# Kernel tuning notes

Measured on AMD Instinct MI355X. Metric: run time of the kernel, lower is better.

## Reference

```python
import jax, jax.numpy as jnp
import numpy as np

N = 100000
E = 1250000
D = 64
R = 16


def _glorot(key, shape):
    fan_in, fan_out = shape[-2], shape[-1]
    lim = jnp.sqrt(6.0 / (fan_in + fan_out))
    return jax.random.uniform(key, shape, jnp.float32, -lim, lim)


def setup_inputs() -> dict:
    key = jax.random.key(0)
    ks = jax.random.split(key, 9)
    x = jax.random.normal(ks[0], (N, D), jnp.float32)
    edge_index = jax.random.randint(ks[1], (2, E), 0, N, jnp.int64 if jax.config.jax_enable_x64 else jnp.int32).astype(jnp.int32)
    edge_type = jax.random.randint(ks[2], (E,), 0, R).astype(jnp.int32)
    return {
        "x": x,
        "edge_index": edge_index,
        "edge_type": edge_type,
        "W1": _glorot(ks[3], (R, D, D)),
        "sw1": _glorot(ks[4], (D, D)),
        "b1": jnp.zeros((D,), jnp.float32),
        "W2": _glorot(ks[5], (R, D, D)),
        "sw2": _glorot(ks[6], (D, D)),
        "b2": jnp.zeros((D,), jnp.float32),
    }


def _rgcn_layer(x, src, dst, edge_type, W, sw, b, residual):
    # self transform [N, O]
    out = x @ sw
    # per-relation transform of all nodes: [N, R, O] (avoids [E, D, O] gathered weights,
    # same math as bmm(x_j, W[edge_type]))
    xW = jnp.einsum('nd,rdo->nro', x, W)
    msg = xW[src, edge_type]                      # [E, O] per-edge messages
    agg = jax.ops.segment_sum(msg, dst, num_segments=N)  # scatter-add aggregate
    out = out + agg
    if residual:
        out = out + x  # Identity residual (in == out channels)
    out = out + b
    return jax.nn.relu(out)


def reference(x, edge_index, edge_type, W1, sw1, b1, W2, sw2, b2):
    src, dst = edge_index[0], edge_index[1]
    # layer 1: residual=True; layer 2: encoding=False -> no residual.
    # activation (relu) applied after every layer by RGCN.forward; dropout p=0 / eval -> no-op.
    h = _rgcn_layer(x, src, dst, edge_type, W1, sw1, b1, residual=True)
    h = _rgcn_layer(h, src, dst, edge_type, W2, sw2, b2, residual=False)
    return h
```

## Files before the change

### kernel.cpp

```cpp
#include <hip/hip_runtime.h>
#include <hip/hip_bf16.h>

#define NN 100000
#define NE 1250000
#define DD 64
#define RR 16
#define NTILE 6250
#define NBINS 100000
#define NBLK_SCAN 391
#define EBCAP 512
#define CLCAP 24

typedef __attribute__((ext_vector_type(8))) short s16x8;
typedef __attribute__((ext_vector_type(4))) float f32x4;

static __device__ __forceinline__ unsigned short f2bf(float v) {
    __hip_bfloat16 h = __float2bfloat16(v);
    return __builtin_bit_cast(unsigned short, h);
}
static __device__ __forceinline__ unsigned int pack2(float a, float b) {
    return ((unsigned int)f2bf(b) << 16) | (unsigned int)f2bf(a);
}


__global__ void hist_key(const int* __restrict__ dst, const int* __restrict__ et,
                         int* __restrict__ cnt) {
    int e = blockIdx.x * 256 + threadIdx.x;
    if (e < NE) atomicAdd(&cnt[(dst[e] >> 4) * 16 + et[e]], 1);
}

__global__ __launch_bounds__(256) void scan1(const int* __restrict__ cnt,
                                             int* __restrict__ rp, int* __restrict__ part) {
    __shared__ int s[256];
    int i = blockIdx.x * 256 + threadIdx.x;
    int v = (i < NBINS) ? cnt[i] : 0;
    s[threadIdx.x] = v;
    __syncthreads();
    for (int off = 1; off < 256; off <<= 1) {
        int t = (threadIdx.x >= off) ? s[threadIdx.x - off] : 0;
        __syncthreads();
        s[threadIdx.x] += t;
        __syncthreads();
    }
    if (i < NBINS) rp[i] = s[threadIdx.x] - v;
    if (threadIdx.x == 255) part[blockIdx.x] = s[255];
}

__global__ void scan2(int* __restrict__ part, int* __restrict__ rp) {
    __shared__ int s[NBLK_SCAN];
    if (threadIdx.x < NBLK_SCAN) s[threadIdx.x] = part[threadIdx.x];
    __syncthreads();
    if (threadIdx.x == 0) {
        int acc = 0;
        for (int b = 0; b < NBLK_SCAN; ++b) { int t = s[b]; s[b] = acc; acc += t; }
        rp[NBINS] = NE;
    }
    __syncthreads();
    if (threadIdx.x < NBLK_SCAN) part[threadIdx.x] = s[threadIdx.x];
}

__global__ void scan3(int* __restrict__ rp, const int* __restrict__ part, int* __restrict__ cur) {
    int i = blockIdx.x * 256 + threadIdx.x;
    if (i < NBINS) {
        int v = rp[i] + part[blockIdx.x];
        rp[i] = v;
        cur[i] = v;
    }
}

__global__ void scatter_key(const int* __restrict__ src, const int* __restrict__ dst,
                            const int* __restrict__ et, int* __restrict__ cur,
                            unsigned int* __restrict__ ep) {
    int e = blockIdx.x * 256 + threadIdx.x;
    if (e >= NE) return;
    int d = dst[e];
    int p = atomicAdd(&cur[(d >> 4) * 16 + et[e]], 1);
    ep[p] = (unsigned int)src[e] | ((unsigned int)(d & 15) << 20);
}


__global__ void prep_w2(const float* __restrict__ W1, const float* __restrict__ sw1,
                        const float* __restrict__ W2, const float* __restrict__ sw2,
                        unsigned short* __restrict__ wt) {
    int i = blockIdx.x * 256 + threadIdx.x;
    if (i >= 2 * 17 * DD * DD) return;
    int d = i & 63;
    int o = (i >> 6) & 63;
    int p = (i >> 12) % 17;
    int l = i / (17 * DD * DD);
    const float* srcp;
    if (p < 16) srcp = (l ? W2 : W1) + p * DD * DD;
    else        srcp = (l ? sw2 : sw1);
    wt[i] = f2bf(srcp[d * DD + o]);
}

__global__ void prep_x2(const float* __restrict__ x, unsigned short* __restrict__ xb) {
    int i = blockIdx.x * blockDim.x + threadIdx.x;
    if (i < NN * DD) xb[i] = f2bf(x[i]);
}


static __device__ __forceinline__ void load_chunk(
    const unsigned short* __restrict__ xb,
    const unsigned int* __restrict__ esrc, int ebase,
    int b0, int s1, int c, int q,
    s16x8& aA0, s16x8& aA1, s16x8& aB0, s16x8& aB1,
    int& dlA, int& dlB, bool& hasB)
{
    hasB = (s1 - b0) > 16;
    int eA = min(b0 + c, s1 - 1);
    unsigned int wa = esrc[eA - ebase];
    int srcA = (int)(wa & 0xFFFFF);
    dlA = (b0 + c < s1) ? (int)(wa >> 20) : 31;
    const unsigned short* xrA = xb + (size_t)srcA * DD + q * 8;
    aA0 = *(const s16x8*)(xrA);
    aA1 = *(const s16x8*)(xrA + 32);
    dlB = 31;
    if (hasB) {
        int eB = min(b0 + 16 + c, s1 - 1);
        unsigned int wb = esrc[eB - ebase];
        int srcB = (int)(wb & 0xFFFFF);
        dlB = (b0 + 16 + c < s1) ? (int)(wb >> 20) : 31;
        const unsigned short* xrB = xb + (size_t)srcB * DD + q * 8;
        aB0 = *(const s16x8*)(xrB);
        aB1 = *(const s16x8*)(xrB + 32);
    } else {
        aB0 = aA0;
        aB1 = aA1;
    }
}

static __device__ __forceinline__ void compute_chunk4(
    const unsigned short* __restrict__ wt, int r, int c, int q,
    const s16x8& aA0, const s16x8& aA1, const s16x8& aB0, const s16x8& aB1,
    int dlA, int dlB, bool hasB, f32x4* D)
{
    s16x8 a2;
    #pragma unroll
    for (int j = 0; j < 4; ++j) {
        int dj = __shfl(dlA, q * 4 + j, 64);
        a2[j] = (dj == c) ? (short)0x3F80 : (short)0;
    }
    #pragma unroll
    for (int j = 0; j < 4; ++j) {
        int dj = hasB ? __shfl(dlB, q * 4 + j, 64) : 31;
        a2[j + 4] = (dj == c) ? (short)0x3F80 : (short)0;
    }
    #pragma unroll
    for (int ob = 0; ob < 4; ++ob) {
        const unsigned short* wrow = wt + r * (DD * DD) + (ob * 16 + c) * DD + q * 8;
        s16x8 w0 = *(const s16x8*)(wrow);
        s16x8 w1 = *(const s16x8*)(wrow + 32);
        f32x4 cA = {0.f, 0.f, 0.f, 0.f};
        cA = __builtin_amdgcn_mfma_f32_16x16x32_bf16(aA0, w0, cA, 0, 0, 0);
        cA = __builtin_amdgcn_mfma_f32_16x16x32_bf16(aA1, w1, cA, 0, 0, 0);
        s16x8 b2;
        if (hasB) {
            f32x4 cB = {0.f, 0.f, 0.f, 0.f};
            cB = __builtin_amdgcn_mfma_f32_16x16x32_bf16(aB0, w0, cB, 0, 0, 0);
            cB = __builtin_amdgcn_mfma_f32_16x16x32_bf16(aB1, w1, cB, 0, 0, 0);
            #pragma unroll
            for (int j = 0; j < 4; ++j) {
                b2[j]     = (short)f2bf(cA[j]);
                b2[j + 4] = (short)f2bf(cB[j]);
            }
        } else {
            #pragma unroll
            for (int j = 0; j < 4; ++j) {
                b2[j]     = (short)f2bf(cA[j]);
                b2[j + 4] = 0;
            }
        }
        D[ob] = __builtin_amdgcn_mfma_f32_16x16x32_bf16(a2, b2, D[ob], 0, 0, 0);
    }
}

__global__ __launch_bounds__(256) void fused_layer(
    const unsigned short* __restrict__ xb,
    const unsigned short* __restrict__ wt,
    const int* __restrict__ rp,
    const unsigned int* __restrict__ ep,
    const float* __restrict__ bias,
    const float* __restrict__ xres,
    unsigned short* __restrict__ outb,
    float* __restrict__ outf)
{
    __shared__ unsigned int eb[EBCAP];
    __shared__ int rps[17];
    __shared__ float Dred[4 * 1024];
    __shared__ int clist[4][CLCAP];
    __shared__ int cmeta[4][3];
    const int tid  = threadIdx.x;
    const int wid  = tid >> 6;
    const int lane = tid & 63;
    const int c = lane & 15;
    const int q = lane >> 4;
    const int tile = blockIdx.x;
    const int n0 = tile * 16;

    const int e0 = rp[tile * 16];
    const int cnt = rp[tile * 16 + 16] - e0;
    if (tid < 17) rps[tid] = rp[tile * 16 + tid];
    const bool inLds = (cnt <= EBCAP);
    {
        const int nst = min(cnt, EBCAP);
        for (int i = tid; i < nst; i += 256) eb[i] = ep[e0 + i];
    }
    __syncthreads();

    if (lane == 0) {
        int m = 0;
        int ovr = -1, ovb = 0;
        for (int rr = wid; rr < 16 && ovr < 0; rr += 4) {
            for (int b0 = rps[rr]; b0 < rps[rr + 1]; b0 += 32) {
                if (m < CLCAP) clist[wid][m++] = (rr << 27) | (b0 - e0);
                else { ovr = rr; ovb = b0; break; }
            }
        }
        cmeta[wid][0] = m;
        cmeta[wid][1] = ovr;
        cmeta[wid][2] = ovb;
    }
    __syncthreads();

    const unsigned int* esrc = inLds ? eb : (ep + e0);
    f32x4 D[4];
    #pragma unroll
    for (int ob = 0; ob < 4; ++ob) D[ob] = (f32x4){0.f, 0.f, 0.f, 0.f};
    const int m = cmeta[wid][0];

    s16x8 aA0, aA1, aB0, aB1;
    int dlA = 31, dlB = 31;
    bool hB = false;
    int rC = 0;
    if (m > 0) {
        int meta = clist[wid][0];
        rC = meta >> 27;
        int b0 = e0 + (meta & 0x7FFFFFF);
        load_chunk(xb, esrc, e0, b0, rps[rC + 1], c, q, aA0, aA1, aB0, aB1, dlA, dlB, hB);
    }
    for (int ci = 0; ci < m; ++ci) {
        s16x8 nA0, nA1, nB0, nB1;
        int ndlA = 31, ndlB = 31;
        bool nhB = false;
        int rN = 0;
        if (ci + 1 < m) {
            int meta = clist[wid][ci + 1];
            rN = meta >> 27;
            int b0 = e0 + (meta & 0x7FFFFFF);
            load_chunk(xb, esrc, e0, b0, rps[rN + 1], c, q, nA0, nA1, nB0, nB1, ndlA, ndlB, nhB);
        }
        compute_chunk4(wt, rC, c, q, aA0, aA1, aB0, aB1, dlA, dlB, hB, D);
        aA0 = nA0; aA1 = nA1; aB0 = nB0; aB1 = nB1;
        dlA = ndlA; dlB = ndlB; hB = nhB; rC = rN;
    }

    {
        const int orr = cmeta[wid][1];
        if (orr >= 0) {
            for (int rr = orr; rr < 16; rr += 4) {
                const int bst = (rr == orr) ? cmeta[wid][2] : rps[rr];
                const int s1 = rps[rr + 1];
                for (int b0 = bst; b0 < s1; b0 += 32) {
                    s16x8 tA0, tA1, tB0, tB1;
                    int tdlA, tdlB;
                    bool thB;
                    load_chunk(xb, esrc, e0, b0, s1, c, q, tA0, tA1, tB0, tB1, tdlA, tdlB, thB);
                    compute_chunk4(wt, rr, c, q, tA0, tA1, tB0, tB1, tdlA, tdlB, thB, D);
                }
            }
        }
    }

    if (wid == 0) {
        const unsigned short* xr = xb + (size_t)(n0 + c) * DD + q * 8;
        s16x8 a0 = *(const s16x8*)(xr);
        s16x8 a1 = *(const s16x8*)(xr + 32);
        s16x8 a2;
        #pragma unroll
        for (int j = 0; j < 4; ++j) {
            a2[j]     = (q * 4 + j == c) ? (short)0x3F80 : (short)0;
            a2[j + 4] = 0;
        }
        #pragma unroll
        for (int ob = 0; ob < 4; ++ob) {
            const unsigned short* wrow = wt + 16 * (DD * DD) + (ob * 16 + c) * DD + q * 8;
            s16x8 w0 = *(const s16x8*)(wrow);
            s16x8 w1 = *(const s16x8*)(wrow + 32);
            f32x4 cA = {0.f, 0.f, 0.f, 0.f};
            cA = __builtin_amdgcn_mfma_f32_16x16x32_bf16(a0, w0, cA, 0, 0, 0);
            cA = __builtin_amdgcn_mfma_f32_16x16x32_bf16(a1, w1, cA, 0, 0, 0);
            s16x8 b2;
            #pragma unroll
            for (int j = 0; j < 4; ++j) {
                b2[j]     = (short)f2bf(cA[j]);
                b2[j + 4] = 0;
            }
            D[ob] = __builtin_amdgcn_mfma_f32_16x16x32_bf16(a2, b2, D[ob], 0, 0, 0);
        }
    }

    {
        float* dred = Dred + wid * 1024;
        #pragma unroll
        for (int ob = 0; ob < 4; ++ob)
            #pragma unroll
            for (int v = 0; v < 4; ++v)
                dred[(q * 4 + v) * 64 + ob * 16 + c] = D[ob][v];
    }
    __syncthreads();

    #pragma unroll
    for (int k = 0; k < 2; ++k) {
        int j = k * 512 + tid * 2;
        int node = j >> 6, ch = j & 63;
        float v0 = Dred[j]        + Dred[1024 + j]     + Dred[2048 + j]     + Dred[3072 + j];
        float v1 = Dred[j + 1]    + Dred[1024 + j + 1] + Dred[2048 + j + 1] + Dred[3072 + j + 1];
        v0 += bias[ch];
        v1 += bias[ch + 1];
        if (xres) {
            const float2 rv = *(const float2*)(xres + (size_t)(n0 + node) * DD + ch);
            v0 += rv.x; v1 += rv.y;
        }
        v0 = fmaxf(v0, 0.f);
        v1 = fmaxf(v1, 0.f);
        if (outb)
            *(unsigned int*)(outb + (size_t)(n0 + node) * DD + ch) = pack2(v0, v1);
        if (outf) {
            float2 o = {v0, v1};
            *(float2*)(outf + (size_t)(n0 + node) * DD + ch) = o;
        }
    }
}


extern "C" void kernel_launch(void* const* d_in, const int* in_sizes, int n_in,
                              void* d_out, int out_size, void* d_ws, size_t ws_size,
                              hipStream_t stream)
{
    (void)in_sizes; (void)n_in; (void)out_size; (void)ws_size;
    const float* x    = (const float*)d_in[0];
    const int*   ei   = (const int*)d_in[1];
    const int*   et   = (const int*)d_in[2];
    const float* W1   = (const float*)d_in[3];
    const float* sw1  = (const float*)d_in[4];
    const float* b1   = (const float*)d_in[5];
    const float* W2   = (const float*)d_in[6];
    const float* sw2  = (const float*)d_in[7];
    const float* b2   = (const float*)d_in[8];
    float* out = (float*)d_out;

    const int* srcA = ei;
    const int* dstA = ei + NE;

    char* ws = (char*)d_ws;
    unsigned short* xb   = (unsigned short*)(ws);
    unsigned short* h1b  = (unsigned short*)(ws + 12800000);
    unsigned short* wt2  = (unsigned short*)(ws + 25600000);
    unsigned int*   ep   = (unsigned int*)(ws + 25878528);
    int*            rp   = (int*)(ws + 30878528);
    int*            cnt  = (int*)(ws + 31278544);
    int*            cur  = (int*)(ws + 31678544);
    int*            part = (int*)(ws + 32078544);

    const int NB_E    = (NE + 255) / 256;
    const int NB_ELEM = (NN * DD + 255) / 256;
    const int WPL = 17 * DD * DD;

    hipMemsetAsync(cnt, 0, NBINS * sizeof(int), stream);
    hist_key<<<NB_E, 256, 0, stream>>>(dstA, et, cnt);
    scan1<<<NBLK_SCAN, 256, 0, stream>>>(cnt, rp, part);
    scan2<<<1, 512, 0, stream>>>(part, rp);
    scan3<<<NBLK_SCAN, 256, 0, stream>>>(rp, part, cur);
    scatter_key<<<NB_E, 256, 0, stream>>>(srcA, dstA, et, cur, ep);

    prep_w2<<<(2 * 17 * DD * DD + 255) / 256, 256, 0, stream>>>(W1, sw1, W2, sw2, wt2);
    prep_x2<<<NB_ELEM, 256, 0, stream>>>(x, xb);

    fused_layer<<<NTILE, 256, 0, stream>>>(xb, wt2, rp, ep, b1, x, h1b, nullptr);
    fused_layer<<<NTILE, 256, 0, stream>>>(h1b, wt2 + WPL, rp, ep, b2, nullptr, nullptr, out);
}
```

Baseline: 530.0 us.

## Use 8 waves per tile and drop software-pipelined chunk list

```diff
diff --git a/kernel.cpp b/kernel.cpp
--- a/kernel.cpp
+++ b/kernel.cpp
@@ -9,7 +9,6 @@
 #define NBINS 100000
 #define NBLK_SCAN 391
 #define EBCAP 512
-#define CLCAP 24
 
 typedef __attribute__((ext_vector_type(8))) short s16x8;
 typedef __attribute__((ext_vector_type(4))) float f32x4;
@@ -175,7 +174,7 @@
     }
 }
 
-__global__ __launch_bounds__(256) void fused_layer(
+__global__ __launch_bounds__(512, 8) void fused_layer(
     const unsigned short* __restrict__ xb,
     const unsigned short* __restrict__ wt,
     const int* __restrict__ rp,
@@ -187,9 +186,7 @@
 {
     __shared__ unsigned int eb[EBCAP];
     __shared__ int rps[17];
-    __shared__ float Dred[4 * 1024];
-    __shared__ int clist[4][CLCAP];
-    __shared__ int cmeta[4][3];
+    __shared__ float Dred[8 * 1024];
     const int tid  = threadIdx.x;
     const int wid  = tid >> 6;
     const int lane = tid & 63;
@@ -204,22 +201,7 @@
     const bool inLds = (cnt <= EBCAP);
     {
         const int nst = min(cnt, EBCAP);
-        for (int i = tid; i < nst; i += 256) eb[i] = ep[e0 + i];
-    }
-    __syncthreads();
-
-    if (lane == 0) {
-        int m = 0;
-        int ovr = -1, ovb = 0;
-        for (int rr = wid; rr < 16 && ovr < 0; rr += 4) {
-            for (int b0 = rps[rr]; b0 < rps[rr + 1]; b0 += 32) {
-                if (m < CLCAP) clist[wid][m++] = (rr << 27) | (b0 - e0);
-                else { ovr = rr; ovb = b0; break; }
-            }
-        }
-        cmeta[wid][0] = m;
-        cmeta[wid][1] = ovr;
-        cmeta[wid][2] = ovb;
+        for (int i = tid; i < nst; i += 512) eb[i] = ep[e0 + i];
     }
     __syncthreads();
 
@@ -227,48 +209,16 @@
     f32x4 D[4];
     #pragma unroll
     for (int ob = 0; ob < 4; ++ob) D[ob] = (f32x4){0.f, 0.f, 0.f, 0.f};
-    const int m = cmeta[wid][0];
-
-    s16x8 aA0, aA1, aB0, aB1;
-    int dlA = 31, dlB = 31;
-    bool hB = false;
-    int rC = 0;
-    if (m > 0) {
-        int meta = clist[wid][0];
-        rC = meta >> 27;
-        int b0 = e0 + (meta & 0x7FFFFFF);
-        load_chunk(xb, esrc, e0, b0, rps[rC + 1], c, q, aA0, aA1, aB0, aB1, dlA, dlB, hB);
-    }
-    for (int ci = 0; ci < m; ++ci) {
-        s16x8 nA0, nA1, nB0, nB1;
-        int ndlA = 31, ndlB = 31;
-        bool nhB = false;
-        int rN = 0;
-        if (ci + 1 < m) {
-            int meta = clist[wid][ci + 1];
-            rN = meta >> 27;
-            int b0 = e0 + (meta & 0x7FFFFFF);
-            load_chunk(xb, esrc, e0, b0, rps[rN + 1], c, q, nA0, nA1, nB0, nB1, ndlA, ndlB, nhB);
-        }
-        compute_chunk4(wt, rC, c, q, aA0, aA1, aB0, aB1, dlA, dlB, hB, D);
-        aA0 = nA0; aA1 = nA1; aB0 = nB0; aB1 = nB1;
-        dlA = ndlA; dlB = ndlB; hB = nhB; rC = rN;
-    }
-
-    {
-        const int orr = cmeta[wid][1];
-        if (orr >= 0) {
-            for (int rr = orr; rr < 16; rr += 4) {
-                const int bst = (rr == orr) ? cmeta[wid][2] : rps[rr];
-                const int s1 = rps[rr + 1];
-                for (int b0 = bst; b0 < s1; b0 += 32) {
-                    s16x8 tA0, tA1, tB0, tB1;
-                    int tdlA, tdlB;
-                    bool thB;
-                    load_chunk(xb, esrc, e0, b0, s1, c, q, tA0, tA1, tB0, tB1, tdlA, tdlB, thB);
-                    compute_chunk4(wt, rr, c, q, tA0, tA1, tB0, tB1, tdlA, tdlB, thB, D);
-                }
-            }
+
+    for (int r = wid; r < 16; r += 8) {
+        const int s0 = rps[r];
+        const int s1 = rps[r + 1];
+        for (int b0 = s0; b0 < s1; b0 += 32) {
+            s16x8 aA0, aA1, aB0, aB1;
+            int dlA, dlB;
+            bool hB;
+            load_chunk(xb, esrc, e0, b0, s1, c, q, aA0, aA1, aB0, aB1, dlA, dlB, hB);
+            compute_chunk4(wt, r, c, q, aA0, aA1, aB0, aB1, dlA, dlB, hB, D);
         }
     }
 
@@ -310,12 +260,15 @@
     }
     __syncthreads();
 
-    #pragma unroll
-    for (int k = 0; k < 2; ++k) {
-        int j = k * 512 + tid * 2;
-        int node = j >> 6, ch = j & 63;
-        float v0 = Dred[j]        + Dred[1024 + j]     + Dred[2048 + j]     + Dred[3072 + j];
-        float v1 = Dred[j + 1]    + Dred[1024 + j + 1] + Dred[2048 + j + 1] + Dred[3072 + j + 1];
+    {
+        const int j = tid * 2;
+        const int node = j >> 6, ch = j & 63;
+        float v0 = 0.f, v1 = 0.f;
+        #pragma unroll
+        for (int p = 0; p < 8; ++p) {
+            v0 += Dred[p * 1024 + j];
+            v1 += Dred[p * 1024 + j + 1];
+        }
         v0 += bias[ch];
         v1 += bias[ch + 1];
         if (xres) {
@@ -377,6 +330,6 @@
     prep_w2<<<(2 * 17 * DD * DD + 255) / 256, 256, 0, stream>>>(W1, sw1, W2, sw2, wt2);
     prep_x2<<<NB_ELEM, 256, 0, stream>>>(x, xb);
 
-    fused_layer<<<NTILE, 256, 0, stream>>>(xb, wt2, rp, ep, b1, x, h1b, nullptr);
-    fused_layer<<<NTILE, 256, 0, stream>>>(h1b, wt2 + WPL, rp, ep, b2, nullptr, nullptr, out);
-}
+    fused_layer<<<NTILE, 512, 0, stream>>>(xb, wt2, rp, ep, b1, x, h1b, nullptr);
+    fused_layer<<<NTILE, 512, 0, stream>>>(h1b, wt2 + WPL, rp, ep, b2, nullptr, nullptr, out);
+}
```

Result: slower. 936.3 us (+76.7%).
